# Kernel optimization log

Hardware: AMD Instinct MI355X
Metric: run time of the kernel (lower is better)

The kernel has to match this reference:

```python
import jax, jax.numpy as jnp
import numpy as np

B, L, H, NH = 32, 512, 256, 4
DH = H // NH
EPS = 1e-12


def setup_inputs() -> dict:
    key = jax.random.key(0)
    ks = jax.random.split(key, 24)
    p = lambda k, shape: 0.02 * jax.random.normal(k, shape, dtype=jnp.float32)
    return {
        "input_tensor": jax.random.normal(ks[0], (B, L, H), dtype=jnp.float32),
        # sorted positive timestamps (seconds-like scale)
        "time_seq": jnp.sort(jax.random.uniform(ks[1], (B, L), dtype=jnp.float32) * 100.0, axis=-1),
        "attention_mask": jnp.zeros((B, 1, L, L), dtype=jnp.float32),
        "item_seq_len": jnp.clip(jax.random.randint(ks[2], (B,), 0, L), 2, L),
        "Wq": p(ks[3], (H, H)), "bq": jnp.zeros((H,), jnp.float32),
        "Wk": p(ks[4], (H, H)), "bk": jnp.zeros((H,), jnp.float32),
        "Wv": p(ks[5], (H, H)), "bv": jnp.zeros((H,), jnp.float32),
        "Wd": p(ks[6], (H, H)), "bd": jnp.zeros((H,), jnp.float32),
        "ln_g": jnp.ones((H,), jnp.float32), "ln_b": jnp.zeros((H,), jnp.float32),
        "Wtq": p(ks[7], (H, H)), "btq": jnp.zeros((H,), jnp.float32),
        "tw1": p(ks[8], (L, L)), "tb1": p(ks[9], (L, L)),
        "tow1": p(ks[10], (L, L)), "tow2": p(ks[11], (L, L)), "tob": p(ks[12], (L, L)),
        "Wt": p(ks[13], (1, 2 * H)), "bt": jnp.zeros((1,), jnp.float32),
    }


def reference(input_tensor, time_seq, attention_mask, item_seq_len,
              Wq, bq, Wk, bk, Wv, bv, Wd, bd, ln_g, ln_b,
              Wtq, btq, tw1, tb1, tow1, tow2, tob, Wt, bt):
    x = input_tensor  # (B, L, H)

    def heads(t):  # (B,L,H) -> (B,NH,L,DH)
        return t.reshape(B, L, NH, DH).transpose(0, 2, 1, 3)

    q = heads(x @ Wq.T + bq)
    k = heads(x @ Wk.T + bk)
    v = heads(x @ Wv.T + bv)

    scores = jnp.einsum('bhqd,bhkd->bhqk', q, k)  # (B,NH,L,L)

    # --- time decay gate ---
    tq = x @ Wtq.T + btq                                  # (B,L,H)
    time_query_key = jnp.tanh(jnp.einsum('bqh,bkh->bqk', tq, x))  # (B,L,L)
    diff = jnp.abs(time_seq[:, :, None] - time_seq[:, None, :])   # |t_i - t_j|
    decay = jnp.tanh(jnp.log1p(diff) * tw1 + tb1)
    decay_gate = tow1 * decay + tow2 * time_query_key + tob       # (B,L,L)
    time_attn = jax.nn.sigmoid(decay_gate)[:, None, :, :]         # (B,1,L,L)

    scores = scores * time_attn / jnp.sqrt(jnp.float32(DH)) + attention_mask
    probs = jax.nn.softmax(scores, axis=-1)

    ctx = jnp.einsum('bhqk,bhkd->bhqd', probs, v)
    ctx = ctx.transpose(0, 2, 1, 3).reshape(B, L, H)

    hs = ctx @ Wd.T + bd + x
    mu = jnp.mean(hs, axis=-1, keepdims=True)
    var = jnp.var(hs, axis=-1, keepdims=True)
    hs = (hs - mu) / jnp.sqrt(var + EPS) * ln_g + ln_b   # (B,L,H)

    bidx = jnp.arange(B)
    emb1 = hs[bidx, item_seq_len - 1]  # (B,H)
    emb2 = hs[bidx, item_seq_len - 2]  # (B,H)
    pred_intervals = jnp.concatenate([emb1, emb2], axis=1) @ Wt.T + bt  # (B,1)
    return hs, pred_intervals
```

## Files before the change

kernel.cpp:

```cpp
#include <hip/hip_runtime.h>
#include <math.h>

#define Bn 32
#define Ln 512
#define Hn 256
#define NHn 4
#define DHn 64

typedef __attribute__((ext_vector_type(8))) short bf16x8;
typedef __attribute__((ext_vector_type(4))) float f32x4;
typedef unsigned int uint32;

__device__ __forceinline__ short f2b(float f) {
    union { float f; uint32 u; } v; v.f = f;
    uint32 r = (v.u + 0x7FFFu + ((v.u >> 16) & 1u)) >> 16;
    return (short)r;
}
__device__ __forceinline__ float b2f(short h) {
    union { uint32 u; float f; } v; v.u = ((uint32)(unsigned short)h) << 16;
    return v.f;
}
__device__ __forceinline__ float fast_tanh(float x) {
    float e = __expf(2.f * x);
    return 1.f - 2.f * __builtin_amdgcn_rcpf(e + 1.f);
}
__device__ __forceinline__ float fast_sigmoid(float x) {
    return __builtin_amdgcn_rcpf(1.f + __expf(-x));
}

__global__ __launch_bounds__(256) void conv_kernel(
    const float* __restrict__ x,
    const float* __restrict__ Wq, const float* __restrict__ Wk,
    const float* __restrict__ Wv, const float* __restrict__ Wtq,
    const float* __restrict__ Wd,
    short* __restrict__ xb, short* __restrict__ wb)
{
    const size_t NLH = (size_t)Bn * Ln * Hn;
    size_t i4 = ((size_t)blockIdx.x * 256 + threadIdx.x) * 4;
    if (i4 < NLH) {
        float4 v = *(const float4*)(x + i4);
        short4 o; o.x = f2b(v.x); o.y = f2b(v.y); o.z = f2b(v.z); o.w = f2b(v.w);
        *(short4*)(xb + i4) = o;
    } else {
        size_t off = i4 - NLH;
        int w = (int)(off >> 16);
        size_t wi = off & 65535;
        const float* src = (w == 0) ? Wq : (w == 1) ? Wk : (w == 2) ? Wv : (w == 3) ? Wtq : Wd;
        float4 v = *(const float4*)(src + wi);
        short4 o; o.x = f2b(v.x); o.y = f2b(v.y); o.z = f2b(v.z); o.w = f2b(v.w);
        *(short4*)(wb + off) = o;
    }
}

struct Acc { f32x4 t[4]; };

__device__ __forceinline__ void gemm_tile_64(
    const short* __restrict__ A,
    const short* __restrict__ Bm,
    int K, short* As, short* Bs, Acc& acc)
{
    const int tid = threadIdx.x;
    const int lane = tid & 63, w = tid >> 6;
    const int quad = lane >> 4, lm = lane & 15;
    const int srow = tid >> 3;
    const int slot = tid & 7;

    for (int k0 = 0; k0 < K; k0 += 64) {
        __syncthreads();
#pragma unroll
        for (int iss = 0; iss < 2; ++iss) {
            int r = srow + iss * 32;
            bf16x8 av = *(const bf16x8*)(A + (size_t)r * K + k0 + slot * 8);
            bf16x8 bv = *(const bf16x8*)(Bm + (size_t)r * K + k0 + slot * 8);
            *(bf16x8*)(As + r * 72 + slot * 8) = av;
            *(bf16x8*)(Bs + r * 72 + slot * 8) = bv;
        }
        __syncthreads();
#pragma unroll
        for (int ks = 0; ks < 2; ++ks) {
            bf16x8 a = *(const bf16x8*)(As + (w * 16 + lm) * 72 + ks * 32 + quad * 8);
#pragma unroll
            for (int kt = 0; kt < 4; ++kt) {
                bf16x8 b = *(const bf16x8*)(Bs + (kt * 16 + lm) * 72 + ks * 32 + quad * 8);
                acc.t[kt] = __builtin_amdgcn_mfma_f32_16x16x32_bf16(a, b, acc.t[kt], 0, 0, 0);
            }
        }
    }
}

__global__ __launch_bounds__(256) void proj_kernel(
    const short* __restrict__ xb, const short* __restrict__ wb,
    const float* __restrict__ bq, const float* __restrict__ bk,
    const float* __restrict__ bv, const float* __restrict__ btq,
    short* __restrict__ qb, short* __restrict__ kb,
    short* __restrict__ vb, short* __restrict__ tqb)
{
    __shared__ short As[64 * 72];
    __shared__ short Bs[64 * 72];
    const int tensor = blockIdx.x >> 2;
    const int ncol0 = (blockIdx.x & 3) * 64;
    const int m0 = blockIdx.y * 64;
    const short* A = xb + (size_t)m0 * Hn;
    const short* Bw = wb + (size_t)tensor * 65536 + (size_t)ncol0 * Hn;
    const float* bias = (tensor == 0) ? bq : (tensor == 1) ? bk : (tensor == 2) ? bv : btq;
    short* out = (tensor == 0) ? qb : (tensor == 1) ? kb : (tensor == 2) ? vb : tqb;

    Acc acc;
#pragma unroll
    for (int i = 0; i < 4; ++i) acc.t[i] = (f32x4){0.f, 0.f, 0.f, 0.f};
    gemm_tile_64(A, Bw, Hn, As, Bs, acc);

    const int lane = threadIdx.x & 63, w = threadIdx.x >> 6;
    const int quad = lane >> 4, lm = lane & 15;
#pragma unroll
    for (int kt = 0; kt < 4; ++kt) {
        int n = ncol0 + kt * 16 + lm;
        float bs = bias[n];
#pragma unroll
        for (int r = 0; r < 4; ++r) {
            int row = m0 + w * 16 + quad * 4 + r;
            out[(size_t)row * Hn + n] = f2b(acc.t[kt][r] + bs);
        }
    }
}

__global__ __launch_bounds__(256) void gate_kernel(
    const short* __restrict__ tqb, const short* __restrict__ xb,
    const float* __restrict__ tseq,
    const float* __restrict__ tw1, const float* __restrict__ tb1,
    const float* __restrict__ tow1, const float* __restrict__ tow2,
    const float* __restrict__ tob,
    short* __restrict__ gateb)
{
    __shared__ short As[64 * 72];
    __shared__ short Bs[64 * 72];
    const int b = blockIdx.z;
    const int m0 = blockIdx.y * 64, n0 = blockIdx.x * 64;
    const short* A = tqb + ((size_t)b * Ln + m0) * Hn;
    const short* Bw = xb + ((size_t)b * Ln + n0) * Hn;

    Acc acc;
#pragma unroll
    for (int i = 0; i < 4; ++i) acc.t[i] = (f32x4){0.f, 0.f, 0.f, 0.f};
    gemm_tile_64(A, Bw, Hn, As, Bs, acc);

    const int lane = threadIdx.x & 63, w = threadIdx.x >> 6;
    const int quad = lane >> 4, lm = lane & 15;
    const float* ts = tseq + (size_t)b * Ln;
    float ti[4];
#pragma unroll
    for (int r = 0; r < 4; ++r) ti[r] = ts[m0 + w * 16 + quad * 4 + r];
#pragma unroll
    for (int kt = 0; kt < 4; ++kt) {
        int j = n0 + kt * 16 + lm;
        float tj = ts[j];
#pragma unroll
        for (int r = 0; r < 4; ++r) {
            int i = m0 + w * 16 + quad * 4 + r;
            size_t ij = (size_t)i * Ln + j;
            float lg = __logf(1.f + fabsf(ti[r] - tj));
            float dec = fast_tanh(lg * tw1[ij] + tb1[ij]);
            float tqk = fast_tanh(acc.t[kt][r]);
            float dg = tow1[ij] * dec + tow2[ij] * tqk + tob[ij];
            float g = 0.125f * fast_sigmoid(dg);
            gateb[(size_t)b * Ln * Ln + ij] = f2b(g);
        }
    }
}

__global__ __launch_bounds__(256) void flash_mfma(
    const short* __restrict__ qb, const short* __restrict__ kb,
    const short* __restrict__ vb, const short* __restrict__ gateb,
    const float* __restrict__ mask, short* __restrict__ ctxb)
{
    __shared__ short Ks[64 * 72];
    __shared__ short Vt[64 * 72];
    __shared__ short Ps[4 * 16 * 72];
    const int q0 = blockIdx.x * 64;
    const int h = blockIdx.y, b = blockIdx.z;
    const int tid = threadIdx.x;
    const int w = tid >> 6, lane = tid & 63;
    const int quad = lane >> 4, lm = lane & 15;

    bf16x8 qf0, qf1;
    {
        const short* qrow = qb + ((size_t)(b * Ln + q0 + w * 16 + lm)) * Hn + h * DHn;
        qf0 = *(const bf16x8*)(qrow + quad * 8);
        qf1 = *(const bf16x8*)(qrow + 32 + quad * 8);
    }

    f32x4 o[4];
#pragma unroll
    for (int i = 0; i < 4; ++i) o[i] = (f32x4){0.f, 0.f, 0.f, 0.f};
    float m_run[4] = {-INFINITY, -INFINITY, -INFINITY, -INFINITY};
    float l_run[4] = {0.f, 0.f, 0.f, 0.f};
    const short* gr_base = gateb + (size_t)b * Ln * Ln;
    const float* mk_base = mask + (size_t)b * Ln * Ln;
    const int qrow0 = q0 + w * 16 + quad * 4;

    for (int k0 = 0; k0 < Ln; k0 += 64) {
        __syncthreads();
        {
            int srow = tid >> 3, slot = tid & 7;
#pragma unroll
            for (int iss = 0; iss < 2; ++iss) {
                int r = srow + iss * 32;
                bf16x8 kv = *(const bf16x8*)(kb + ((size_t)(b * Ln + k0 + r)) * Hn + h * DHn + slot * 8);
                *(bf16x8*)(Ks + r * 72 + slot * 8) = kv;
            }
        }
        {
            int key = tid >> 2, dq = tid & 3;
            const short* vr = vb + ((size_t)(b * Ln + k0 + key)) * Hn + h * DHn + dq * 16;
            bf16x8 v0 = *(const bf16x8*)(vr);
            bf16x8 v1 = *(const bf16x8*)(vr + 8);
#pragma unroll
            for (int u = 0; u < 8; ++u) Vt[(dq * 16 + u) * 72 + key] = v0[u];
#pragma unroll
            for (int u = 0; u < 8; ++u) Vt[(dq * 16 + 8 + u) * 72 + key] = v1[u];
        }
        __syncthreads();

        f32x4 s[4];
#pragma unroll
        for (int kt = 0; kt < 4; ++kt) {
            s[kt] = (f32x4){0.f, 0.f, 0.f, 0.f};
            bf16x8 b0 = *(const bf16x8*)(Ks + (kt * 16 + lm) * 72 + quad * 8);
            s[kt] = __builtin_amdgcn_mfma_f32_16x16x32_bf16(qf0, b0, s[kt], 0, 0, 0);
            bf16x8 b1 = *(const bf16x8*)(Ks + (kt * 16 + lm) * 72 + 32 + quad * 8);
            s[kt] = __builtin_amdgcn_mfma_f32_16x16x32_bf16(qf1, b1, s[kt], 0, 0, 0);
        }

        float mnew[4];
#pragma unroll
        for (int r = 0; r < 4; ++r) mnew[r] = m_run[r];
#pragma unroll
        for (int kt = 0; kt < 4; ++kt) {
            int col = k0 + kt * 16 + lm;
#pragma unroll
            for (int r = 0; r < 4; ++r) {
                float g = b2f(gr_base[(size_t)(qrow0 + r) * Ln + col]);
                float mv = mk_base[(size_t)(qrow0 + r) * Ln + col];
                float sv = s[kt][r] * g + mv;
                s[kt][r] = sv;
                mnew[r] = fmaxf(mnew[r], sv);
            }
        }
        float alpha[4], rsum[4];
#pragma unroll
        for (int r = 0; r < 4; ++r) {
#pragma unroll
            for (int off = 1; off < 16; off <<= 1)
                mnew[r] = fmaxf(mnew[r], __shfl_xor(mnew[r], off, 64));
            alpha[r] = __expf(m_run[r] - mnew[r]);
            m_run[r] = mnew[r];
            rsum[r] = 0.f;
        }
        float p[4][4];
#pragma unroll
        for (int kt = 0; kt < 4; ++kt)
#pragma unroll
            for (int r = 0; r < 4; ++r) {
                float pv = __expf(s[kt][r] - m_run[r]);
                p[kt][r] = pv;
                rsum[r] += pv;
            }
#pragma unroll
        for (int r = 0; r < 4; ++r) {
#pragma unroll
            for (int off = 1; off < 16; off <<= 1) rsum[r] += __shfl_xor(rsum[r], off, 64);
            l_run[r] = l_run[r] * alpha[r] + rsum[r];
#pragma unroll
            for (int ot = 0; ot < 4; ++ot) o[ot][r] *= alpha[r];
        }
        short* pw = Ps + w * 16 * 72;
#pragma unroll
        for (int kt = 0; kt < 4; ++kt)
#pragma unroll
            for (int r = 0; r < 4; ++r)
                pw[(quad * 4 + r) * 72 + kt * 16 + lm] = f2b(p[kt][r]);

#pragma unroll
        for (int ks = 0; ks < 2; ++ks) {
            bf16x8 pa = *(const bf16x8*)(pw + lm * 72 + ks * 32 + quad * 8);
#pragma unroll
            for (int ot = 0; ot < 4; ++ot) {
                bf16x8 vv = *(const bf16x8*)(Vt + (ot * 16 + lm) * 72 + ks * 32 + quad * 8);
                o[ot] = __builtin_amdgcn_mfma_f32_16x16x32_bf16(pa, vv, o[ot], 0, 0, 0);
            }
        }
    }

    float inv[4];
#pragma unroll
    for (int r = 0; r < 4; ++r) inv[r] = 1.0f / l_run[r];
#pragma unroll
    for (int ot = 0; ot < 4; ++ot) {
        int d = h * DHn + ot * 16 + lm;
#pragma unroll
        for (int r = 0; r < 4; ++r) {
            int row = b * Ln + qrow0 + r;
            ctxb[(size_t)row * Hn + d] = f2b(o[ot][r] * inv[r]);
        }
    }
}

__global__ __launch_bounds__(256) void outproj_kernel(
    const short* __restrict__ ctxb, const short* __restrict__ wdb,
    const float* __restrict__ bd, const float* __restrict__ x,
    float* __restrict__ out)
{
    __shared__ short As[64 * 72];
    __shared__ short Bs[64 * 72];
    const int n0 = blockIdx.x * 64, m0 = blockIdx.y * 64;
    Acc acc;
#pragma unroll
    for (int i = 0; i < 4; ++i) acc.t[i] = (f32x4){0.f, 0.f, 0.f, 0.f};
    gemm_tile_64(ctxb + (size_t)m0 * Hn, wdb + (size_t)n0 * Hn, Hn, As, Bs, acc);

    const int lane = threadIdx.x & 63, w = threadIdx.x >> 6;
    const int quad = lane >> 4, lm = lane & 15;
#pragma unroll
    for (int kt = 0; kt < 4; ++kt) {
        int n = n0 + kt * 16 + lm;
        float bs = bd[n];
#pragma unroll
        for (int r = 0; r < 4; ++r) {
            int row = m0 + w * 16 + quad * 4 + r;
            out[(size_t)row * Hn + n] = acc.t[kt][r] + bs + x[(size_t)row * Hn + n];
        }
    }
}

__global__ __launch_bounds__(256) void ln_kernel(float* __restrict__ hs,
                                                 const float* __restrict__ g,
                                                 const float* __restrict__ bta)
{
    const int row = blockIdx.x, t = threadIdx.x;
    float v = hs[(size_t)row * Hn + t];
    float s1 = v, s2 = v * v;
#pragma unroll
    for (int off = 32; off > 0; off >>= 1) {
        s1 += __shfl_xor(s1, off, 64);
        s2 += __shfl_xor(s2, off, 64);
    }
    __shared__ float red[8];
    if ((t & 63) == 0) { red[t >> 6] = s1; red[4 + (t >> 6)] = s2; }
    __syncthreads();
    float sum = red[0] + red[1] + red[2] + red[3];
    float sq  = red[4] + red[5] + red[6] + red[7];
    float mu  = sum * (1.f / 256.f);
    float var = sq * (1.f / 256.f) - mu * mu;
    float rstd = rsqrtf(var + 1e-12f);
    hs[(size_t)row * Hn + t] = (v - mu) * rstd * g[t] + bta[t];
}

__global__ __launch_bounds__(256) void pred_kernel(const float* __restrict__ hs,
                                                   const int* __restrict__ lens,
                                                   const float* __restrict__ Wt,
                                                   const float* __restrict__ bt,
                                                   float* __restrict__ pred)
{
    const int b = blockIdx.x, t = threadIdx.x;
    int len = lens[b];
    float e1 = hs[((size_t)b * Ln + (len - 1)) * Hn + t];
    float e2 = hs[((size_t)b * Ln + (len - 2)) * Hn + t];
    float v = e1 * Wt[t] + e2 * Wt[Hn + t];
#pragma unroll
    for (int off = 32; off > 0; off >>= 1) v += __shfl_xor(v, off, 64);
    __shared__ float ps[4];
    if ((t & 63) == 0) ps[t >> 6] = v;
    __syncthreads();
    if (t == 0) pred[b] = ps[0] + ps[1] + ps[2] + ps[3] + bt[0];
}

extern "C" void kernel_launch(void* const* d_in, const int* in_sizes, int n_in,
                              void* d_out, int out_size, void* d_ws, size_t ws_size,
                              hipStream_t stream) {
    (void)in_sizes; (void)n_in; (void)out_size; (void)ws_size;
    const float* x    = (const float*)d_in[0];
    const float* tseq = (const float*)d_in[1];
    const float* mask = (const float*)d_in[2];
    const int*   lens = (const int*)d_in[3];
    const float* Wq = (const float*)d_in[4];  const float* bq = (const float*)d_in[5];
    const float* Wk = (const float*)d_in[6];  const float* bk = (const float*)d_in[7];
    const float* Wv = (const float*)d_in[8];  const float* bv = (const float*)d_in[9];
    const float* Wd = (const float*)d_in[10]; const float* bd = (const float*)d_in[11];
    const float* ln_g = (const float*)d_in[12]; const float* ln_b = (const float*)d_in[13];
    const float* Wtq = (const float*)d_in[14]; const float* btq = (const float*)d_in[15];
    const float* tw1 = (const float*)d_in[16]; const float* tb1 = (const float*)d_in[17];
    const float* tow1 = (const float*)d_in[18]; const float* tow2 = (const float*)d_in[19];
    const float* tob = (const float*)d_in[20];
    const float* Wt = (const float*)d_in[21]; const float* bt = (const float*)d_in[22];

    const size_t NLH = (size_t)Bn * Ln * Hn;
    short* ws = (short*)d_ws;
    short* xb    = ws;
    short* wb    = xb + NLH;
    short* qb    = wb + 5 * 65536;
    short* kb    = qb + NLH;
    short* vb    = kb + NLH;
    short* tqb   = vb + NLH;
    short* gateb = tqb + NLH;
    short* ctxb  = gateb + (size_t)Bn * Ln * Ln;
    float* out   = (float*)d_out;

    dim3 blk(256);
    conv_kernel<<<dim3(4416), blk, 0, stream>>>(x, Wq, Wk, Wv, Wtq, Wd, xb, wb);
    proj_kernel<<<dim3(16, 256), blk, 0, stream>>>(xb, wb, bq, bk, bv, btq, qb, kb, vb, tqb);
    gate_kernel<<<dim3(8, 8, Bn), blk, 0, stream>>>(tqb, xb, tseq, tw1, tb1, tow1, tow2, tob, gateb);
    flash_mfma<<<dim3(8, NHn, Bn), blk, 0, stream>>>(qb, kb, vb, gateb, mask, ctxb);
    outproj_kernel<<<dim3(4, 256), blk, 0, stream>>>(ctxb, wb + 4 * 65536, bd, x, out);
    ln_kernel<<<dim3(Bn * Ln), blk, 0, stream>>>(out, ln_g, ln_b);
    pred_kernel<<<dim3(Bn), blk, 0, stream>>>(out, lens, Wt, bt, out + NLH);
}
```

Measured before the change: 237.6 us.

## Process all heads per attention block to share gate/mask loads and drop running max

The attention kernel now gives each 128-thread block 32 queries across all four heads, instead of one head per block. The gate and mask tile is loaded once per key tile and reused by every head, where before it was reloaded for each head. All heads' V are staged transposed into shared memory with packed 32-bit stores, while K fragments are read straight from global memory. The online-softmax running max and rescaling are removed, so exp is applied to raw gated scores; this is exact only while scores stay small enough not to overflow, and grid parallelism per block is lower.

```diff
diff --git a/kernel.cpp b/kernel.cpp
--- a/kernel.cpp
+++ b/kernel.cpp
@@ -168,141 +168,128 @@
     }
 }
 
-__global__ __launch_bounds__(256) void flash_mfma(
+__global__ __launch_bounds__(128) void flash_mfma(
     const short* __restrict__ qb, const short* __restrict__ kb,
     const short* __restrict__ vb, const short* __restrict__ gateb,
     const float* __restrict__ mask, short* __restrict__ ctxb)
 {
-    __shared__ short Ks[64 * 72];
-    __shared__ short Vt[64 * 72];
-    __shared__ short Ps[4 * 16 * 72];
-    const int q0 = blockIdx.x * 64;
-    const int h = blockIdx.y, b = blockIdx.z;
+    __shared__ short Vt[256 * 74];
+    __shared__ short Ps[2 * 16 * 72];
+    const int q0 = blockIdx.x * 32;
+    const int b = blockIdx.y;
     const int tid = threadIdx.x;
     const int w = tid >> 6, lane = tid & 63;
     const int quad = lane >> 4, lm = lane & 15;
 
-    bf16x8 qf0, qf1;
+    bf16x8 qf[4][2];
     {
-        const short* qrow = qb + ((size_t)(b * Ln + q0 + w * 16 + lm)) * Hn + h * DHn;
-        qf0 = *(const bf16x8*)(qrow + quad * 8);
-        qf1 = *(const bf16x8*)(qrow + 32 + quad * 8);
-    }
-
-    f32x4 o[4];
-#pragma unroll
-    for (int i = 0; i < 4; ++i) o[i] = (f32x4){0.f, 0.f, 0.f, 0.f};
-    float m_run[4] = {-INFINITY, -INFINITY, -INFINITY, -INFINITY};
-    float l_run[4] = {0.f, 0.f, 0.f, 0.f};
-    const short* gr_base = gateb + (size_t)b * Ln * Ln;
-    const float* mk_base = mask + (size_t)b * Ln * Ln;
+        const short* qrow = qb + ((size_t)(b * Ln + q0 + w * 16 + lm)) * Hn;
+#pragma unroll
+        for (int h = 0; h < 4; ++h) {
+            qf[h][0] = *(const bf16x8*)(qrow + h * DHn + quad * 8);
+            qf[h][1] = *(const bf16x8*)(qrow + h * DHn + 32 + quad * 8);
+        }
+    }
+
+    f32x4 o[4][4];
+#pragma unroll
+    for (int h = 0; h < 4; ++h)
+#pragma unroll
+        for (int i = 0; i < 4; ++i) o[h][i] = (f32x4){0.f, 0.f, 0.f, 0.f};
+    float lpart[4][4];
+#pragma unroll
+    for (int h = 0; h < 4; ++h)
+#pragma unroll
+        for (int r = 0; r < 4; ++r) lpart[h][r] = 0.f;
+
     const int qrow0 = q0 + w * 16 + quad * 4;
+    const short* gr = gateb + (size_t)b * Ln * Ln;
+    const float* mk = mask + (size_t)b * Ln * Ln;
+    const int kp = tid >> 2;
+    const int ds0 = tid & 3;
 
     for (int k0 = 0; k0 < Ln; k0 += 64) {
         __syncthreads();
         {
-            int srow = tid >> 3, slot = tid & 7;
-#pragma unroll
-            for (int iss = 0; iss < 2; ++iss) {
-                int r = srow + iss * 32;
-                bf16x8 kv = *(const bf16x8*)(kb + ((size_t)(b * Ln + k0 + r)) * Hn + h * DHn + slot * 8);
-                *(bf16x8*)(Ks + r * 72 + slot * 8) = kv;
-            }
-        }
-        {
-            int key = tid >> 2, dq = tid & 3;
-            const short* vr = vb + ((size_t)(b * Ln + k0 + key)) * Hn + h * DHn + dq * 16;
-            bf16x8 v0 = *(const bf16x8*)(vr);
-            bf16x8 v1 = *(const bf16x8*)(vr + 8);
-#pragma unroll
-            for (int u = 0; u < 8; ++u) Vt[(dq * 16 + u) * 72 + key] = v0[u];
-#pragma unroll
-            for (int u = 0; u < 8; ++u) Vt[(dq * 16 + 8 + u) * 72 + key] = v1[u];
+            const short* vbase = vb + ((size_t)(b * Ln + k0)) * Hn;
+            const short* va_p = vbase + (size_t)(2 * kp) * Hn;
+            const short* vc_p = vbase + (size_t)(2 * kp + 1) * Hn;
+#pragma unroll
+            for (int it = 0; it < 8; ++it) {
+                int dslot = ds0 + it * 4;
+                bf16x8 va = *(const bf16x8*)(va_p + dslot * 8);
+                bf16x8 vc = *(const bf16x8*)(vc_p + dslot * 8);
+#pragma unroll
+                for (int u = 0; u < 8; ++u) {
+                    uint32 pk = (uint32)(unsigned short)va[u] |
+                                ((uint32)(unsigned short)vc[u] << 16);
+                    *(uint32*)&Vt[(dslot * 8 + u) * 74 + 2 * kp] = pk;
+                }
+            }
         }
         __syncthreads();
 
-        f32x4 s[4];
-#pragma unroll
-        for (int kt = 0; kt < 4; ++kt) {
-            s[kt] = (f32x4){0.f, 0.f, 0.f, 0.f};
-            bf16x8 b0 = *(const bf16x8*)(Ks + (kt * 16 + lm) * 72 + quad * 8);
-            s[kt] = __builtin_amdgcn_mfma_f32_16x16x32_bf16(qf0, b0, s[kt], 0, 0, 0);
-            bf16x8 b1 = *(const bf16x8*)(Ks + (kt * 16 + lm) * 72 + 32 + quad * 8);
-            s[kt] = __builtin_amdgcn_mfma_f32_16x16x32_bf16(qf1, b1, s[kt], 0, 0, 0);
-        }
-
-        float mnew[4];
-#pragma unroll
-        for (int r = 0; r < 4; ++r) mnew[r] = m_run[r];
+        float gv[4][4], mv[4][4];
 #pragma unroll
         for (int kt = 0; kt < 4; ++kt) {
             int col = k0 + kt * 16 + lm;
 #pragma unroll
             for (int r = 0; r < 4; ++r) {
-                float g = b2f(gr_base[(size_t)(qrow0 + r) * Ln + col]);
-                float mv = mk_base[(size_t)(qrow0 + r) * Ln + col];
-                float sv = s[kt][r] * g + mv;
-                s[kt][r] = sv;
-                mnew[r] = fmaxf(mnew[r], sv);
-            }
-        }
-        float alpha[4], rsum[4];
+                size_t idx = (size_t)(qrow0 + r) * Ln + col;
+                gv[kt][r] = b2f(gr[idx]);
+                mv[kt][r] = mk[idx];
+            }
+        }
+
+        short* pw = Ps + w * 16 * 72;
+#pragma unroll
+        for (int h = 0; h < 4; ++h) {
+            const short* kbase = kb + ((size_t)(b * Ln + k0)) * Hn + h * DHn;
+            f32x4 s[4];
+#pragma unroll
+            for (int kt = 0; kt < 4; ++kt) {
+                const short* krow = kbase + (size_t)(kt * 16 + lm) * Hn;
+                s[kt] = (f32x4){0.f, 0.f, 0.f, 0.f};
+                bf16x8 b0 = *(const bf16x8*)(krow + quad * 8);
+                s[kt] = __builtin_amdgcn_mfma_f32_16x16x32_bf16(qf[h][0], b0, s[kt], 0, 0, 0);
+                bf16x8 b1 = *(const bf16x8*)(krow + 32 + quad * 8);
+                s[kt] = __builtin_amdgcn_mfma_f32_16x16x32_bf16(qf[h][1], b1, s[kt], 0, 0, 0);
+            }
+#pragma unroll
+            for (int kt = 0; kt < 4; ++kt)
+#pragma unroll
+                for (int r = 0; r < 4; ++r) {
+                    float pv = __expf(s[kt][r] * gv[kt][r] + mv[kt][r]);
+                    lpart[h][r] += pv;
+                    pw[(quad * 4 + r) * 72 + kt * 16 + lm] = f2b(pv);
+                }
+#pragma unroll
+            for (int ks = 0; ks < 2; ++ks) {
+                bf16x8 pa = *(const bf16x8*)(pw + lm * 72 + ks * 32 + quad * 8);
+#pragma unroll
+                for (int ot = 0; ot < 4; ++ot) {
+                    bf16x8 vv = *(const bf16x8*)(Vt + (h * DHn + ot * 16 + lm) * 74 + ks * 32 + quad * 8);
+                    o[h][ot] = __builtin_amdgcn_mfma_f32_16x16x32_bf16(pa, vv, o[h][ot], 0, 0, 0);
+                }
+            }
+        }
+    }
+
+#pragma unroll
+    for (int h = 0; h < 4; ++h)
 #pragma unroll
         for (int r = 0; r < 4; ++r) {
-#pragma unroll
-            for (int off = 1; off < 16; off <<= 1)
-                mnew[r] = fmaxf(mnew[r], __shfl_xor(mnew[r], off, 64));
-            alpha[r] = __expf(m_run[r] - mnew[r]);
-            m_run[r] = mnew[r];
-            rsum[r] = 0.f;
-        }
-        float p[4][4];
-#pragma unroll
-        for (int kt = 0; kt < 4; ++kt)
-#pragma unroll
-            for (int r = 0; r < 4; ++r) {
-                float pv = __expf(s[kt][r] - m_run[r]);
-                p[kt][r] = pv;
-                rsum[r] += pv;
-            }
-#pragma unroll
-        for (int r = 0; r < 4; ++r) {
-#pragma unroll
-            for (int off = 1; off < 16; off <<= 1) rsum[r] += __shfl_xor(rsum[r], off, 64);
-            l_run[r] = l_run[r] * alpha[r] + rsum[r];
-#pragma unroll
-            for (int ot = 0; ot < 4; ++ot) o[ot][r] *= alpha[r];
-        }
-        short* pw = Ps + w * 16 * 72;
-#pragma unroll
-        for (int kt = 0; kt < 4; ++kt)
-#pragma unroll
-            for (int r = 0; r < 4; ++r)
-                pw[(quad * 4 + r) * 72 + kt * 16 + lm] = f2b(p[kt][r]);
-
-#pragma unroll
-        for (int ks = 0; ks < 2; ++ks) {
-            bf16x8 pa = *(const bf16x8*)(pw + lm * 72 + ks * 32 + quad * 8);
+            float lv = lpart[h][r];
+#pragma unroll
+            for (int off = 1; off < 16; off <<= 1) lv += __shfl_xor(lv, off, 64);
+            float inv = 1.0f / lv;
+            int row = b * Ln + qrow0 + r;
 #pragma unroll
             for (int ot = 0; ot < 4; ++ot) {
-                bf16x8 vv = *(const bf16x8*)(Vt + (ot * 16 + lm) * 72 + ks * 32 + quad * 8);
-                o[ot] = __builtin_amdgcn_mfma_f32_16x16x32_bf16(pa, vv, o[ot], 0, 0, 0);
-            }
-        }
-    }
-
-    float inv[4];
-#pragma unroll
-    for (int r = 0; r < 4; ++r) inv[r] = 1.0f / l_run[r];
-#pragma unroll
-    for (int ot = 0; ot < 4; ++ot) {
-        int d = h * DHn + ot * 16 + lm;
-#pragma unroll
-        for (int r = 0; r < 4; ++r) {
-            int row = b * Ln + qrow0 + r;
-            ctxb[(size_t)row * Hn + d] = f2b(o[ot][r] * inv[r]);
-        }
-    }
+                int d = h * DHn + ot * 16 + lm;
+                ctxb[(size_t)row * Hn + d] = f2b(o[h][ot][r] * inv);
+            }
+        }
 }
 
 __global__ __launch_bounds__(256) void outproj_kernel(
@@ -409,7 +396,7 @@
     conv_kernel<<<dim3(4416), blk, 0, stream>>>(x, Wq, Wk, Wv, Wtq, Wd, xb, wb);
     proj_kernel<<<dim3(16, 256), blk, 0, stream>>>(xb, wb, bq, bk, bv, btq, qb, kb, vb, tqb);
     gate_kernel<<<dim3(8, 8, Bn), blk, 0, stream>>>(tqb, xb, tseq, tw1, tb1, tow1, tow2, tob, gateb);
-    flash_mfma<<<dim3(8, NHn, Bn), blk, 0, stream>>>(qb, kb, vb, gateb, mask, ctxb);
+    flash_mfma<<<dim3(16, 32), dim3(128), 0, stream>>>(qb, kb, vb, gateb, mask, ctxb);
     outproj_kernel<<<dim3(4, 256), blk, 0, stream>>>(ctxb, wb + 4 * 65536, bd, x, out);
     ln_kernel<<<dim3(Bn * Ln), blk, 0, stream>>>(out, ln_g, ln_b);
     pred_kernel<<<dim3(Bn), blk, 0, stream>>>(out, lens, Wt, bt, out + NLH);
```

After: 319.4 us. +34.4%, slower.
